# Optimization experiments

Measured on AMD Instinct MI355X. Metric: run time of the kernel, lower is better.

Reference implementation:

```python
import jax, jax.numpy as jnp
import numpy as np

UNITS, ORDER, THETA, DT = 512, 256, 784.0, 1.0


def _lmu_AB(order, theta, dt):
    # Continuous-time Legendre delay system (Voelker & Eliasmith 2018)
    Q = np.arange(order, dtype=np.float64)
    R = (2.0 * Q + 1.0)[:, None] / theta
    i, j = np.meshgrid(Q, Q, indexing='ij')
    A = np.where(i < j, -1.0, (-1.0) ** (i - j + 1)) * R
    B = ((-1.0) ** Q)[:, None] * R
    # ZOH discretization: Ad = expm(A*dt); Bd = A^{-1}(Ad - I)B
    Ad = np.asarray(jax.scipy.linalg.expm(jnp.asarray(A * dt, dtype=jnp.float64)))
    Bd = np.linalg.solve(A, (Ad - np.eye(order)) @ B)
    # cell stores AT = (Ad - I)^T so that m <- m + m@AT + u@BT
    return (Ad - np.eye(order)).T.astype(np.float32), Bd.T.astype(np.float32)


def setup_inputs() -> dict:
    key = jax.random.key(0)
    ks = jax.random.split(key, 6)
    D = 1
    x = jax.random.normal(ks[0], (64, 1024, D), dtype=jnp.float32)
    # lecun_uniform: U(-sqrt(3/fan_in), sqrt(3/fan_in))
    ie = jax.random.uniform(ks[1], (D, 1), minval=-np.sqrt(3.0 / D), maxval=np.sqrt(3.0 / D), dtype=jnp.float32)
    he = jax.random.uniform(ks[2], (UNITS, 1), minval=-np.sqrt(3.0 / UNITS), maxval=np.sqrt(3.0 / UNITS), dtype=jnp.float32)
    me = jnp.zeros((ORDER, 1), dtype=jnp.float32)  # Constant(0) initializer
    # glorot_normal: std = sqrt(2/(fan_in+fan_out))
    ik = jax.random.normal(ks[3], (D, UNITS), dtype=jnp.float32) * np.sqrt(2.0 / (D + UNITS))
    hk = jax.random.normal(ks[4], (UNITS, UNITS), dtype=jnp.float32) * np.sqrt(2.0 / (2 * UNITS))
    mk = jax.random.normal(ks[5], (ORDER, UNITS), dtype=jnp.float32) * np.sqrt(2.0 / (ORDER + UNITS))
    AT, BT = _lmu_AB(ORDER, THETA / DT, DT)
    return {"x": x, "input_encoders": ie, "hidden_encoders": he, "memory_encoders": me,
            "input_kernel": ik, "hidden_kernel": hk, "memory_kernel": mk,
            "AT": jnp.asarray(AT), "BT": jnp.asarray(BT)}


def reference(x, input_encoders, hidden_encoders, memory_encoders,
              input_kernel, hidden_kernel, memory_kernel, AT, BT):
    B = x.shape[0]
    h0 = jnp.zeros((B, UNITS), dtype=x.dtype)
    m0 = jnp.zeros((B, ORDER), dtype=x.dtype)

    def step(carry, xt):  # xt: [B, D]
        h, m = carry
        u = xt @ input_encoders + h @ hidden_encoders + m @ memory_encoders  # [B,1]
        m = m + m @ AT + u @ BT                                             # [B,order]
        h = jnp.tanh(xt @ input_kernel + h @ hidden_kernel + m @ memory_kernel)
        return (h, m), h

    xs = jnp.transpose(x, (1, 0, 2))  # [T,B,D]
    _, hs = jax.lax.scan(step, (h0, m0), xs)
    return jnp.transpose(hs, (1, 0, 2))  # [B,T,units]
```

## Files before the change

### kernel.cpp

```cpp
#include <hip/hip_runtime.h>
#include <hip/hip_fp16.h>

typedef unsigned int u32;
typedef unsigned short u16;
typedef _Float16 half2v __attribute__((ext_vector_type(2)));
typedef u32 u32x4 __attribute__((ext_vector_type(4)));
typedef u32 u32x2 __attribute__((ext_vector_type(2)));

#define N_UNITS 512
#define N_ORDER 256
#define N_T     1024
#define N_B     64
#define KWG     4
#define PKT_STRIDE 288

__device__ inline float dot2f(u32 a, u32 b, float acc) {
    return __builtin_amdgcn_fdot2(__builtin_bit_cast(half2v, a),
                                  __builtin_bit_cast(half2v, b), acc, false);
}
__device__ inline u16 f2h_bits(float v) {
    _Float16 f = (_Float16)v;
    return __builtin_bit_cast(u16, f);
}
__device__ inline float hbits2f(u32 dw) {
    u16 s = (u16)(dw & 0xFFFFu);
    _Float16 f = __builtin_bit_cast(_Float16, s);
    return (float)f;
}
__device__ inline u32 pack_h2(float a, float b) {
    return (u32)f2h_bits(a) | ((u32)f2h_bits(b) << 16);
}
__device__ inline u32 aload(const u32* p) {
    return __hip_atomic_load(p, __ATOMIC_RELAXED, __HIP_MEMORY_SCOPE_AGENT);
}
__device__ inline void astore(u32* p, u32 v) {
    __hip_atomic_store(p, v, __ATOMIC_RELAXED, __HIP_MEMORY_SCOPE_AGENT);
}
__device__ inline u32x4 aload4(const u32* p) {
    u32x4 r;
    asm volatile("global_load_dwordx4 %0, %1, off sc0 sc1\n\ts_waitcnt vmcnt(0)"
                 : "=&v"(r) : "v"(p) : "memory");
    return r;
}
__device__ inline u32x2 aload2(const u32* p) {
    u32x2 r;
    asm volatile("global_load_dwordx2 %0, %1, off sc0 sc1\n\ts_waitcnt vmcnt(0)"
                 : "=&v"(r) : "v"(p) : "memory");
    return r;
}
__device__ inline void astore2(u32* p, u32 a, u32 b) {
    u32x2 v; v.x = a; v.y = b;
    asm volatile("global_store_dwordx2 %0, %1, off sc0 sc1"
                 :: "v"(p), "v"(v) : "memory");
}

__global__ __launch_bounds__(256)
void prep_hk(const float* __restrict__ hk, u32* __restrict__ hk2) {
    int tid = blockIdx.x * 256 + threadIdx.x;
    int kk = tid >> 9, c = tid & 511;
    hk2[tid] = pack_h2(hk[(2 * kk) * 512 + c], hk[(2 * kk + 1) * 512 + c]);
}

__global__ __launch_bounds__(512)
void prep_amk(const float* __restrict__ mk, const float* __restrict__ at,
              const float* __restrict__ bt,
              u32* __restrict__ amk2, float* __restrict__ bmk) {
    int bj = blockIdx.x, c = threadIdx.x;
    if (bj < 128) {
        int j0 = 2 * bj, j1 = j0 + 1;
        float a0 = mk[j0 * 512 + c];
        float a1 = mk[j1 * 512 + c];
        #pragma unroll 8
        for (int k = 0; k < 256; ++k) {
            float w = mk[k * 512 + c];
            a0 = fmaf(at[j0 * 256 + k], w, a0);
            a1 = fmaf(at[j1 * 256 + k], w, a1);
        }
        amk2[bj * 512 + c] = pack_h2(a0, a1);
    } else {
        float s = 0.f;
        #pragma unroll 8
        for (int k = 0; k < 256; ++k) s = fmaf(bt[k], mk[k * 512 + c], s);
        bmk[c] = s;
    }
}

__global__ __launch_bounds__(512, 2)
void lmu_main(const float* __restrict__ x, const float* __restrict__ ie,
              const float* __restrict__ he, const float* __restrict__ me,
              const float* __restrict__ ik, const float* __restrict__ bt,
              const float* __restrict__ at,
              const u32* __restrict__ hk2, const u32* __restrict__ amk2,
              const float* __restrict__ bmk,
              u32* __restrict__ pkt, float* __restrict__ out) {
    __shared__ float xs[N_T];
    __shared__ float he_sl[128], ik_sl[128], bmk_sl[128];
    __shared__ float me_sl[64], bt_sl[64];
    __shared__ __align__(8) u16 h_h16[N_UNITS];
    __shared__ __align__(8) u16 m_hi16[N_ORDER], m_lo16[N_ORDER];
    __shared__ __align__(8) float mf[N_ORDER];
    __shared__ float zbuf[512], ampart[512];
    __shared__ float upart[4];
    __shared__ float upw[2];

    const int tid = threadIdx.x;
    const int g   = blockIdx.x;
    const int b   = g & 63;
    const int q   = g >> 6;
    const int kg  = tid >> 7;
    const int cl  = tid & 127;
    const int kg8 = tid >> 6;
    const int jl  = tid & 63;
    const int J   = 64 * q + jl;
    const int lane = tid & 63;

    for (int i = tid; i < N_T; i += 512) xs[i] = x[b * N_T + i];
    if (tid < 128) {
        he_sl[tid]  = he[128 * q + tid];
        ik_sl[tid]  = ik[128 * q + tid];
        bmk_sl[tid] = bmk[128 * q + tid];
    }
    if (tid < 64) { me_sl[tid] = me[J]; bt_sl[tid] = bt[J]; }
    h_h16[tid] = 0;
    if (tid < 256) { m_hi16[tid] = 0; m_lo16[tid] = 0; mf[tid] = 0.f; }
    if (tid < 4) upart[tid] = 0.f;
    const float ie0 = ie[0];

    u32 hk_w[64];
    #pragma unroll
    for (int i = 0; i < 64; ++i)
        hk_w[i] = hk2[(size_t)(64 * kg + i) * 512 + 128 * q + cl];
    u32 amk_w[32];
    #pragma unroll
    for (int i = 0; i < 32; ++i)
        amk_w[i] = amk2[(size_t)(32 * kg + i) * 512 + 128 * q + cl];
    float at_w[32];
    #pragma unroll
    for (int i = 0; i < 32; ++i)
        at_w[i] = at[(size_t)(32 * kg8 + i) * 256 + J];

    __syncthreads();

    const u32* h2u   = reinterpret_cast<const u32*>(h_h16);
    const u32* m_hi2 = reinterpret_cast<const u32*>(m_hi16);
    const u32* m_lo2 = reinterpret_cast<const u32*>(m_lo16);
    float* outb = out + (size_t)b * N_T * N_UNITS;

    for (int t = 0; t < N_T; ++t) {
        if (t > 0) {
            const u32 ep  = (u32)t;
            const int par = (t - 1) & 1;
            if (tid < 195) {
                int pi = (tid < 192) ? (tid >> 6) : (tid - 192);
                int q2 = pi + (pi >= q ? 1 : 0);
                const u32* base = pkt + (size_t)(par * 256 + b * 4 + q2) * PKT_STRIDE;
                if (tid < 192) {
                    int i = tid & 63;
                    u32 d0, d1, d2, d3;
                    for (;;) {
                        u32x4 dv = aload4(base + 4 * i);
                        d0 = dv.x; d1 = dv.y; d2 = dv.z; d3 = dv.w;
                        if (((((d0 >> 16) ^ ep) | ((d1 >> 16) ^ ep)) |
                             (((d2 >> 16) ^ ep) | ((d3 >> 16) ^ ep))) == 0) break;
                    }
                    if (i < 32) {
                        int idx = 64 * q2 + 2 * i;
                        mf[idx]         = hbits2f(d0) + hbits2f(d1);
                        m_hi16[idx]     = (u16)d0;  m_lo16[idx]     = (u16)d1;
                        mf[idx + 1]     = hbits2f(d2) + hbits2f(d3);
                        m_hi16[idx + 1] = (u16)d2;  m_lo16[idx + 1] = (u16)d3;
                    } else {
                        int idx = 128 * q2 + (4 * i - 128);
                        h_h16[idx]     = (u16)d0;
                        h_h16[idx + 1] = (u16)d1;
                        h_h16[idx + 2] = (u16)d2;
                        h_h16[idx + 3] = (u16)d3;
                    }
                } else {
                    u32 d0, d1;
                    for (;;) {
                        u32x2 dv = aload2(base + 256);
                        d0 = dv.x; d1 = dv.y;
                        if ((((d0 >> 16) ^ ep) | ((d1 >> 16) ^ ep)) == 0) break;
                    }
                    upart[q2] = hbits2f(d0) + hbits2f(d1);
                }
            }
        }
        __syncthreads();

        {
            float z = 0.f;
            #pragma unroll
            for (int i = 0; i < 64; ++i)
                z = dot2f(h2u[64 * kg + i], hk_w[i], z);
            #pragma unroll
            for (int i = 0; i < 32; ++i) {
                u32 w = amk_w[i];
                z = dot2f(m_hi2[32 * kg + i], w, z);
                z = dot2f(m_lo2[32 * kg + i], w, z);
            }
            zbuf[tid] = z;
            float am = 0.f;
            #pragma unroll
            for (int i = 0; i < 32; ++i)
                am = fmaf(mf[32 * kg8 + i], at_w[i], am);
            ampart[tid] = am;
        }
        __syncthreads();

        float u = 0.f, mnew = 0.f, hnew = 0.f;
        u16 mhi_b = 0, mlo_b = 0;
        if (tid < 128)
            u = upart[0] + upart[1] + upart[2] + upart[3] + xs[t] * ie0;
        if (tid < 64) {
            mnew = mf[J] + u * bt_sl[tid];
            #pragma unroll
            for (int gi = 0; gi < 8; ++gi) mnew += ampart[tid + 64 * gi];
            _Float16 hi = (_Float16)mnew;
            float lo = mnew - (float)hi;
            mhi_b = __builtin_bit_cast(u16, hi);
            mlo_b = f2h_bits(lo);
            mf[J] = mnew;
            m_hi16[J] = mhi_b;
            m_lo16[J] = mlo_b;
        }
        if (tid < 128) {
            float zf = zbuf[tid] + zbuf[tid + 128] + zbuf[tid + 256] + zbuf[tid + 384]
                     + xs[t] * ik_sl[tid] + u * bmk_sl[tid];
            hnew = tanhf(zf);
            __builtin_nontemporal_store(hnew, &outb[(size_t)t * N_UNITS + 128 * q + tid]);
            h_h16[128 * q + tid] = f2h_bits(hnew);
        }

        if (t < N_T - 1) {
            const u32 eph = (u32)(t + 1) << 16;
            u32* myb = pkt + (size_t)((t & 1) * 256 + b * 4 + q) * PKT_STRIDE;
            if (tid < 64)
                astore2(myb + 2 * tid, (u32)mhi_b | eph, (u32)mlo_b | eph);
            if (tid < 128)
                astore(myb + 128 + tid, (u32)f2h_bits(hnew) | eph);

            float up = 0.f;
            if (tid < 128) {
                up = hnew * he_sl[tid];
                if (tid < 64) up = fmaf(mnew, me_sl[tid], up);
            }
            #pragma unroll
            for (int off = 32; off > 0; off >>= 1) up += __shfl_down(up, off);
            if (lane == 0 && tid < 128) upw[tid >> 6] = up;
            __syncthreads();
            if (tid == 0) {
                float myu = upw[0] + upw[1];
                upart[q] = myu;
                _Float16 hi = (_Float16)myu;
                float lo = myu - (float)hi;
                astore2(myb + 256, (u32)__builtin_bit_cast(u16, hi) | eph,
                                   (u32)f2h_bits(lo) | eph);
            }
        }
    }
}

extern "C" void kernel_launch(void* const* d_in, const int* in_sizes, int n_in,
                              void* d_out, int out_size, void* d_ws, size_t ws_size,
                              hipStream_t stream) {
    const float* x  = (const float*)d_in[0];
    const float* ie = (const float*)d_in[1];
    const float* he = (const float*)d_in[2];
    const float* me = (const float*)d_in[3];
    const float* ik = (const float*)d_in[4];
    const float* hk = (const float*)d_in[5];
    const float* mk = (const float*)d_in[6];
    const float* at = (const float*)d_in[7];
    const float* bt = (const float*)d_in[8];

    u32*   hk2  = (u32*)d_ws;
    u32*   amk2 = hk2 + 256 * 512;
    float* bmk  = (float*)(amk2 + 128 * 512);
    u32*   pkt  = (u32*)(bmk + 512);

    prep_hk<<<512, 256, 0, stream>>>(hk, hk2);
    prep_amk<<<129, 512, 0, stream>>>(mk, at, bt, amk2, bmk);
    lmu_main<<<N_B * KWG, 512, 0, stream>>>(x, ie, he, me, ik, bt, at,
                                            hk2, amk2, bmk, pkt, (float*)d_out);
}
```

Baseline: 2.760 ms.

## Remove per-step barrier for u partials and widen packet stores

Each of the two wavefronts now writes its own u partial straight into the packet (four dwords instead of two), and u partials are double-buffered by step parity. This removes the extra __syncthreads and the tid==0 serial reduction from every timestep of the recurrent critical path. Packet stores are merged through lane shuffles into dwordx4/dwordx2 writes, and LDS unpacking uses packed 32-bit stores. The cost is more packet payload, one more polled dword, and a parity-based buffering scheme whose correctness depends on barrier ordering across steps.

```diff
diff --git a/kernel.cpp b/kernel.cpp
--- a/kernel.cpp
+++ b/kernel.cpp
@@ -30,27 +30,20 @@
 __device__ inline u32 pack_h2(float a, float b) {
     return (u32)f2h_bits(a) | ((u32)f2h_bits(b) << 16);
 }
-__device__ inline u32 aload(const u32* p) {
-    return __hip_atomic_load(p, __ATOMIC_RELAXED, __HIP_MEMORY_SCOPE_AGENT);
-}
-__device__ inline void astore(u32* p, u32 v) {
-    __hip_atomic_store(p, v, __ATOMIC_RELAXED, __HIP_MEMORY_SCOPE_AGENT);
-}
 __device__ inline u32x4 aload4(const u32* p) {
     u32x4 r;
     asm volatile("global_load_dwordx4 %0, %1, off sc0 sc1\n\ts_waitcnt vmcnt(0)"
                  : "=&v"(r) : "v"(p) : "memory");
     return r;
 }
-__device__ inline u32x2 aload2(const u32* p) {
-    u32x2 r;
-    asm volatile("global_load_dwordx2 %0, %1, off sc0 sc1\n\ts_waitcnt vmcnt(0)"
-                 : "=&v"(r) : "v"(p) : "memory");
-    return r;
-}
 __device__ inline void astore2(u32* p, u32 a, u32 b) {
     u32x2 v; v.x = a; v.y = b;
     asm volatile("global_store_dwordx2 %0, %1, off sc0 sc1"
+                 :: "v"(p), "v"(v) : "memory");
+}
+__device__ inline void astore4(u32* p, u32 a, u32 b, u32 c, u32 d) {
+    u32x4 v; v.x = a; v.y = b; v.z = c; v.w = d;
+    asm volatile("global_store_dwordx4 %0, %1, off sc0 sc1"
                  :: "v"(p), "v"(v) : "memory");
 }
 
@@ -100,8 +93,8 @@
     __shared__ __align__(8) u16 m_hi16[N_ORDER], m_lo16[N_ORDER];
     __shared__ __align__(8) float mf[N_ORDER];
     __shared__ float zbuf[512], ampart[512];
-    __shared__ float upart[4];
-    __shared__ float upw[2];
+    __shared__ float upart[2][4];
+    __shared__ float upw[2][2];
 
     const int tid = threadIdx.x;
     const int g   = blockIdx.x;
@@ -123,7 +116,8 @@
     if (tid < 64) { me_sl[tid] = me[J]; bt_sl[tid] = bt[J]; }
     h_h16[tid] = 0;
     if (tid < 256) { m_hi16[tid] = 0; m_lo16[tid] = 0; mf[tid] = 0.f; }
-    if (tid < 4) upart[tid] = 0.f;
+    if (tid < 8) (&upart[0][0])[tid] = 0.f;
+    if (tid < 4) (&upw[0][0])[tid] = 0.f;
     const float ie0 = ie[0];
 
     u32 hk_w[64];
@@ -147,6 +141,8 @@
     float* outb = out + (size_t)b * N_T * N_UNITS;
 
     for (int t = 0; t < N_T; ++t) {
+        const int pc = t & 1;
+
         if (t > 0) {
             const u32 ep  = (u32)t;
             const int par = (t - 1) & 1;
@@ -165,25 +161,28 @@
                     }
                     if (i < 32) {
                         int idx = 64 * q2 + 2 * i;
-                        mf[idx]         = hbits2f(d0) + hbits2f(d1);
-                        m_hi16[idx]     = (u16)d0;  m_lo16[idx]     = (u16)d1;
-                        mf[idx + 1]     = hbits2f(d2) + hbits2f(d3);
-                        m_hi16[idx + 1] = (u16)d2;  m_lo16[idx + 1] = (u16)d3;
+                        float2 v;
+                        v.x = hbits2f(d0) + hbits2f(d1);
+                        v.y = hbits2f(d2) + hbits2f(d3);
+                        *reinterpret_cast<float2*>(mf + idx) = v;
+                        reinterpret_cast<u32*>(m_hi16)[idx >> 1] = (d0 & 0xFFFFu) | (d2 << 16);
+                        reinterpret_cast<u32*>(m_lo16)[idx >> 1] = (d1 & 0xFFFFu) | (d3 << 16);
                     } else {
-                        int idx = 128 * q2 + (4 * i - 128);
-                        h_h16[idx]     = (u16)d0;
-                        h_h16[idx + 1] = (u16)d1;
-                        h_h16[idx + 2] = (u16)d2;
-                        h_h16[idx + 3] = (u16)d3;
+                        int i0 = (128 * q2 + 4 * i - 128) >> 1;
+                        u32* hhp = reinterpret_cast<u32*>(h_h16);
+                        hhp[i0]     = (d0 & 0xFFFFu) | (d1 << 16);
+                        hhp[i0 + 1] = (d2 & 0xFFFFu) | (d3 << 16);
                     }
                 } else {
-                    u32 d0, d1;
+                    u32 d0, d1, d2, d3;
                     for (;;) {
-                        u32x2 dv = aload2(base + 256);
-                        d0 = dv.x; d1 = dv.y;
-                        if ((((d0 >> 16) ^ ep) | ((d1 >> 16) ^ ep)) == 0) break;
+                        u32x4 dv = aload4(base + 256);
+                        d0 = dv.x; d1 = dv.y; d2 = dv.z; d3 = dv.w;
+                        if (((((d0 >> 16) ^ ep) | ((d1 >> 16) ^ ep)) |
+                             (((d2 >> 16) ^ ep) | ((d3 >> 16) ^ ep))) == 0) break;
                     }
-                    upart[q2] = hbits2f(d0) + hbits2f(d1);
+                    upart[pc][q2] = (hbits2f(d0) + hbits2f(d1))
+                                  + (hbits2f(d2) + hbits2f(d3));
                 }
             }
         }
@@ -212,7 +211,8 @@
         float u = 0.f, mnew = 0.f, hnew = 0.f;
         u16 mhi_b = 0, mlo_b = 0;
         if (tid < 128)
-            u = upart[0] + upart[1] + upart[2] + upart[3] + xs[t] * ie0;
+            u = ((upart[pc][0] + upart[pc][1]) + (upart[pc][2] + upart[pc][3]))
+              + (upw[pc][0] + upw[pc][1]) + xs[t] * ie0;
         if (tid < 64) {
             mnew = mf[J] + u * bt_sl[tid];
             #pragma unroll
@@ -236,10 +236,16 @@
         if (t < N_T - 1) {
             const u32 eph = (u32)(t + 1) << 16;
             u32* myb = pkt + (size_t)((t & 1) * 256 + b * 4 + q) * PKT_STRIDE;
-            if (tid < 64)
-                astore2(myb + 2 * tid, (u32)mhi_b | eph, (u32)mlo_b | eph);
-            if (tid < 128)
-                astore(myb + 128 + tid, (u32)f2h_bits(hnew) | eph);
+            if (tid < 64) {
+                u32 m0 = (u32)mhi_b | eph, m1 = (u32)mlo_b | eph;
+                u32 n0 = __shfl_xor(m0, 1), n1 = __shfl_xor(m1, 1);
+                if ((jl & 1) == 0) astore4(myb + 2 * jl, m0, m1, n0, n1);
+            }
+            if (tid < 128) {
+                u32 hd = (u32)f2h_bits(hnew) | eph;
+                u32 hn = __shfl_xor(hd, 1);
+                if ((tid & 1) == 0) astore2(myb + 128 + tid, hd, hn);
+            }
 
             float up = 0.f;
             if (tid < 128) {
@@ -248,15 +254,13 @@
             }
             #pragma unroll
             for (int off = 32; off > 0; off >>= 1) up += __shfl_down(up, off);
-            if (lane == 0 && tid < 128) upw[tid >> 6] = up;
-            __syncthreads();
-            if (tid == 0) {
-                float myu = upw[0] + upw[1];
-                upart[q] = myu;
-                _Float16 hi = (_Float16)myu;
-                float lo = myu - (float)hi;
-                astore2(myb + 256, (u32)__builtin_bit_cast(u16, hi) | eph,
-                                   (u32)f2h_bits(lo) | eph);
+            if (lane == 0 && tid < 128) {
+                const int w01 = tid >> 6;
+                upw[pc ^ 1][w01] = up;
+                _Float16 hi = (_Float16)up;
+                float lo = up - (float)hi;
+                astore2(myb + 256 + 2 * w01, (u32)__builtin_bit_cast(u16, hi) | eph,
+                                             (u32)f2h_bits(lo) | eph);
             }
         }
     }
```

After: 3.040 ms. 1.1x slower.

## Precompute local-slice partial dot products before waiting on remote packets

Applied to the files above, without the earlier changes.

The hidden-state and memory reductions are split into four slices by source workgroup. The slice produced by the local workgroup is accumulated at the end of the previous step, while packets from peer workgroups are still in flight. After the spin-wait, only the three remote slices are summed. The goal is to shorten the critical path of each timestep; the cost is a new weight interleaving and extra live registers for the early partial sums.

```diff
diff --git a/kernel.cpp b/kernel.cpp
--- a/kernel.cpp
+++ b/kernel.cpp
@@ -128,16 +128,22 @@
 
     u32 hk_w[64];
     #pragma unroll
-    for (int i = 0; i < 64; ++i)
-        hk_w[i] = hk2[(size_t)(64 * kg + i) * 512 + 128 * q + cl];
+    for (int s = 0; s < 4; ++s)
+        #pragma unroll
+        for (int i = 0; i < 16; ++i)
+            hk_w[16 * s + i] = hk2[(size_t)(64 * s + 16 * kg + i) * 512 + 128 * q + cl];
     u32 amk_w[32];
     #pragma unroll
-    for (int i = 0; i < 32; ++i)
-        amk_w[i] = amk2[(size_t)(32 * kg + i) * 512 + 128 * q + cl];
+    for (int s = 0; s < 4; ++s)
+        #pragma unroll
+        for (int i = 0; i < 8; ++i)
+            amk_w[8 * s + i] = amk2[(size_t)(32 * s + 8 * kg + i) * 512 + 128 * q + cl];
     float at_w[32];
     #pragma unroll
-    for (int i = 0; i < 32; ++i)
-        at_w[i] = at[(size_t)(32 * kg8 + i) * 256 + J];
+    for (int s = 0; s < 4; ++s)
+        #pragma unroll
+        for (int i = 0; i < 8; ++i)
+            at_w[8 * s + i] = at[(size_t)(64 * s + 8 * kg8 + i) * 256 + J];
 
     __syncthreads();
 
@@ -145,6 +151,8 @@
     const u32* m_hi2 = reinterpret_cast<const u32*>(m_hi16);
     const u32* m_lo2 = reinterpret_cast<const u32*>(m_lo16);
     float* outb = out + (size_t)b * N_T * N_UNITS;
+
+    float ez = 0.f, eam = 0.f;
 
     for (int t = 0; t < N_T; ++t) {
         if (t > 0) {
@@ -190,21 +198,29 @@
         __syncthreads();
 
         {
-            float z = 0.f;
+            float z = ez;
             #pragma unroll
-            for (int i = 0; i < 64; ++i)
-                z = dot2f(h2u[64 * kg + i], hk_w[i], z);
+            for (int s = 0; s < 4; ++s) {
+                if (s == q) continue;
+                #pragma unroll
+                for (int i = 0; i < 16; ++i)
+                    z = dot2f(h2u[64 * s + 16 * kg + i], hk_w[16 * s + i], z);
+                #pragma unroll
+                for (int i = 0; i < 8; ++i) {
+                    u32 wv = amk_w[8 * s + i];
+                    z = dot2f(m_hi2[32 * s + 8 * kg + i], wv, z);
+                    z = dot2f(m_lo2[32 * s + 8 * kg + i], wv, z);
+                }
+            }
+            zbuf[tid] = z;
+            float am = eam;
             #pragma unroll
-            for (int i = 0; i < 32; ++i) {
-                u32 w = amk_w[i];
-                z = dot2f(m_hi2[32 * kg + i], w, z);
-                z = dot2f(m_lo2[32 * kg + i], w, z);
-            }
-            zbuf[tid] = z;
-            float am = 0.f;
-            #pragma unroll
-            for (int i = 0; i < 32; ++i)
-                am = fmaf(mf[32 * kg8 + i], at_w[i], am);
+            for (int s = 0; s < 4; ++s) {
+                if (s == q) continue;
+                #pragma unroll
+                for (int i = 0; i < 8; ++i)
+                    am = fmaf(mf[64 * s + 8 * kg8 + i], at_w[8 * s + i], am);
+            }
             ampart[tid] = am;
         }
         __syncthreads();
@@ -258,6 +274,33 @@
                 astore2(myb + 256, (u32)__builtin_bit_cast(u16, hi) | eph,
                                    (u32)f2h_bits(lo) | eph);
             }
+
+            #define EARLY_CHUNK(SQ)                                              \
+            {                                                                    \
+                float e = 0.f, ea = 0.f;                                         \
+                _Pragma("unroll")                                                \
+                for (int i = 0; i < 16; ++i)                                     \
+                    e = dot2f(h2u[64 * (SQ) + 16 * kg + i],                      \
+                              hk_w[16 * (SQ) + i], e);                           \
+                _Pragma("unroll")                                                \
+                for (int i = 0; i < 8; ++i) {                                    \
+                    u32 wv = amk_w[8 * (SQ) + i];                                \
+                    e = dot2f(m_hi2[32 * (SQ) + 8 * kg + i], wv, e);             \
+                    e = dot2f(m_lo2[32 * (SQ) + 8 * kg + i], wv, e);             \
+                }                                                                \
+                _Pragma("unroll")                                                \
+                for (int i = 0; i < 8; ++i)                                      \
+                    ea = fmaf(mf[64 * (SQ) + 8 * kg8 + i],                       \
+                              at_w[8 * (SQ) + i], ea);                           \
+                ez = e; eam = ea;                                                \
+            }
+            switch (q) {
+                case 0:  EARLY_CHUNK(0); break;
+                case 1:  EARLY_CHUNK(1); break;
+                case 2:  EARLY_CHUNK(2); break;
+                default: EARLY_CHUNK(3); break;
+            }
+            #undef EARLY_CHUNK
         }
     }
 }
```

Result: faster. 2.675 ms (-3.1%).
